# Kernel tuning notes

Hardware: AMD Instinct MI355X
Metric: run time of the kernel (lower is better)

## Reference

```python
import jax, jax.numpy as jnp
import numpy as np

N = 8192      # points
K = 16        # nsample neighbors
CIN = 64      # in_plane
C = 256       # out_plane (== mid_planes)
S = 8         # share_planes
EPS = 1e-5


def _bn(x, g, b, axes):
    # BatchNorm1d (training-mode batch stats, biased var), channel = last dim
    m = x.mean(axes, keepdims=True)
    v = x.var(axes, keepdims=True)
    return (x - m) / jnp.sqrt(v + EPS) * g + b


def _knn(p, k):
    # brute-force KNN over a single batch (o = [N]); indices include self
    sq = jnp.sum(p * p, axis=1)
    d2 = sq[:, None] + sq[None, :] - 2.0 * (p @ p.T)   # [N, N]
    idx = jax.lax.top_k(-d2, k)[1]                      # [N, K]
    return jax.lax.stop_gradient(idx)


def setup_inputs() -> dict:
    key = jax.random.key(0)
    ks = jax.random.split(key, 16)
    W = lambda i, shp, s=0.05: jax.random.normal(ks[i], shp, jnp.float32) * s
    one = lambda d: jnp.ones((d,), jnp.float32)
    zero = lambda d: jnp.zeros((d,), jnp.float32)
    return {
        "p": jax.random.normal(ks[0], (N, 3), jnp.float32),
        "x": jax.random.normal(ks[1], (N, CIN), jnp.float32),
        "o": jnp.array([N], dtype=jnp.int32),
        # PointAggregation (stride=1): Linear(no bias) + BN
        "W_pa": W(2, (CIN, C)), "g_pa": one(C), "b_pa": zero(C),
        # SelfFusion.linear1 (no bias) + bn1
        "W1": W(3, (C, C)), "g1": one(C), "b1": zero(C),
        # SelfFusionLayer q/k/v
        "Wq": W(4, (C, C)), "bq": zero(C),
        "Wk": W(5, (C, C)), "bk": zero(C),
        "Wv": W(6, (C, C)), "bv": zero(C),
        # linear_p: Linear(3,3)+BN(3)+ReLU+Linear(3,C)
        "Wp1": W(7, (3, 3), 0.3), "bp1": zero(3), "gp": one(3), "bp": zero(3),
        "Wp2": W(8, (3, C), 0.3), "bp2": zero(C),
        # linear_w: BN(C)+ReLU+Linear(C,C//S)+BN(C//S)+ReLU+Linear(C//S,C//S)
        "gw1": one(C), "bw1": zero(C),
        "Ww1": W(9, (C, C // S)), "bww1": zero(C // S),
        "gw2": one(C // S), "bw2": zero(C // S),
        "Ww2": W(10, (C // S, C // S), 0.2), "bww2": zero(C // S),
        # bn2, linear3 (no bias) + bn3
        "g2": one(C), "b2": zero(C),
        "W3": W(11, (C, C)), "g3": one(C), "b3": zero(C),
    }


def reference(p, x, o, W_pa, g_pa, b_pa, W1, g1, b1, Wq, bq, Wk, bk, Wv, bv,
              Wp1, bp1, gp, bp, Wp2, bp2, gw1, bw1, Ww1, bww1, gw2, bw2,
              Ww2, bww2, g2, b2, W3, g3, b3):
    relu = jax.nn.relu
    # --- PointAggregation (stride=1) ---
    h = relu(_bn(x @ W_pa, g_pa, b_pa, (0,)))          # [N, C]
    # --- SelfFusion block ---
    identity = h
    h = relu(_bn(h @ W1, g1, b1, (0,)))                # [N, C]
    # SelfFusionLayer
    xq = h @ Wq + bq                                   # [N, C]
    xk = h @ Wk + bk
    xv = h @ Wv + bv
    idx = _knn(p, K)                                   # [N, K]
    rel = p[idx] - p[:, None, :]                       # [N, K, 3] relative coords
    xk_g = xk[idx]                                     # [N, K, C]
    xv_g = xv[idx]                                     # [N, K, C]
    # linear_p: Linear(3,3) -> BN(3) -> ReLU -> Linear(3,C)
    p_r = rel @ Wp1 + bp1
    p_r = relu(_bn(p_r, gp, bp, (0, 1)))
    p_r = p_r @ Wp2 + bp2                              # [N, K, C]
    # mid_planes == out_planes so view(...).sum(2) is identity
    w = xk_g - xq[:, None, :] + p_r                    # [N, K, C]
    # linear_w: BN -> ReLU -> Linear -> BN -> ReLU -> Linear
    w = relu(_bn(w, gw1, bw1, (0, 1)))
    w = w @ Ww1 + bww1                                 # [N, K, C//S]
    w = relu(_bn(w, gw2, bw2, (0, 1)))
    w = w @ Ww2 + bww2                                 # [N, K, C//S]
    w = jax.nn.softmax(w, axis=1)                      # softmax over neighbors
    y = ((xv_g + p_r).reshape(N, K, S, C // S) * w[:, :, None, :]).sum(1)
    y = y.reshape(N, C)
    # back in SelfFusion
    y = relu(_bn(y, g2, b2, (0,)))
    y = _bn(y @ W3, g3, b3, (0,))
    x2 = relu(y + identity)
    return (p, x2, o)
```

## Files before the change

kernel.cpp:

```cpp
#include <hip/hip_runtime.h>
#include <hip/hip_bf16.h>

#define INV_N  (1.0f/8192.0f)
#define INV_NK (1.0f/131072.0f)

typedef __attribute__((ext_vector_type(8))) short bf16x8;
typedef __attribute__((ext_vector_type(4))) float f32x4;
typedef unsigned short u16;

__device__ __forceinline__ u16 f2b(float f) {
  unsigned u = __float_as_uint(f);
  return (u16)((u + 0x7FFFu + ((u >> 16) & 1u)) >> 16);
}
__device__ __forceinline__ float b2f(u16 u) {
  return __uint_as_float(((unsigned)u) << 16);
}

__device__ __forceinline__ float bn_ap(float v, const float* st, int C, int ch,
                                       float inv, float g, float b) {
  float m = st[ch] * inv;
  float var = st[C + ch] * inv - m * m;
  return (v - m) * rsqrtf(var + 1e-5f) * g + b;
}

// ... 111 lines not shown
  float* lscl = (float*)(smem + 18432);
  float* lsft = (float*)(smem + 19456);
  int t = threadIdx.x;
  int m0 = bm * 64, n0 = bn_ * 64;
  if (BNA) {
    for (int e = t; e < KA; e += 256) {
      float m = st[e] * inv_cnt;
      float var = st[KA + e] * inv_cnt - m*m;
      float sc = rsqrtf(var + 1e-5f) * g[e];
      lscl[e] = sc; lsft[e] = bb[e] - m*sc;
    }
    __syncthreads();
  }
  const f32x4 zero = {0.f, 0.f, 0.f, 0.f};
  f32x4 acc[2][2] = {{zero, zero}, {zero, zero}};
  int wv = t >> 6, l = t & 63;
  int wm = wv & 1, wn = wv >> 1;
  int lr = l & 15, lk = (l >> 4) * 8;
  int ra = t >> 4, qa = t & 15;
  int bn = t & 63, bkc = t >> 6;
  for (int k0 = 0; k0 < KA; k0 += 64) {
#pragma unroll
    for (int rp = 0; rp < 4; ++rp) {
      int r = rp*16 + ra;
      float vv[4];
      if constexpr (sizeof(TA) == 4) {
        float4 av = *(const float4*)((const float*)A + (size_t)(m0 + r)*KA + k0 + qa*4);
        vv[0] = av.x; vv[1] = av.y; vv[2] = av.z; vv[3] = av.w;
      } else {
        short4 av = *(const short4*)((const u16*)A + (size_t)(m0 + r)*KA + k0 + qa*4);
#pragma unroll
        for (int jj = 0; jj < 4; ++jj) vv[jj] = b2f(((u16*)&av)[jj]);
      }
      short4 s;
#pragma unroll
      for (int jj = 0; jj < 4; ++jj) {
        float v = vv[jj];
        if (BNA) { int ch = k0 + qa*4 + jj; v = fmaxf(fmaf(v, lscl[ch], lsft[ch]), 0.f); }
        ((u16*)&s)[jj] = f2b(v);
      }
      *(short4*)&As[r][qa*4] = s;
    }
    {
      float v[16];
#pragma unroll
      for (int j2 = 0; j2 < 16; ++j2)
        v[j2] = W[(size_t)(k0 + bkc*16 + j2)*NOUT + n0 + bn];
      bf16x8 w0, w1v;
#pragma unroll
      for (int j2 = 0; j2 < 8; ++j2) {
        w0[j2]  = (short)f2b(v[j2]);
        w1v[j2] = (short)f2b(v[8 + j2]);
      }
      *(bf16x8*)&Bt[bn][bkc*16]     = w0;
      *(bf16x8*)&Bt[bn][bkc*16 + 8] = w1v;
    }
    __syncthreads();
#pragma unroll
    for (int fk = 0; fk < 2; ++fk) {
      bf16x8 a0 = *(const bf16x8*)&As[wm*32 +      lr][fk*32 + lk];
      bf16x8 a1 = *(const bf16x8*)&As[wm*32 + 16 + lr][fk*32 + lk];
      bf16x8 b0 = *(const bf16x8*)&Bt[wn*32 +      lr][fk*32 + lk];
      bf16x8 b1 = *(const bf16x8*)&Bt[wn*32 + 16 + lr][fk*32 + lk];
      acc[0][0] = __builtin_amdgcn_mfma_f32_16x16x32_bf16(a0, b0, acc[0][0], 0, 0, 0);
      acc[0][1] = __builtin_amdgcn_mfma_f32_16x16x32_bf16(a0, b1, acc[0][1], 0, 0, 0);
      acc[1][0] = __builtin_amdgcn_mfma_f32_16x16x32_bf16(a1, b0, acc[1][0], 0, 0, 0);
      acc[1][1] = __builtin_amdgcn_mfma_f32_16x16x32_bf16(a1, b1, acc[1][1], 0, 0, 0);
    }
    __syncthreads();
  }
#pragma unroll
  for (int fn = 0; fn < 2; ++fn) {
    int col = n0 + wn*32 + fn*16 + lr;
    float s1 = 0.f, s2 = 0.f;
#pragma unroll
    for (int fm = 0; fm < 2; ++fm) {
#pragma unroll
      for (int r = 0; r < 4; ++r) {
        int row = m0 + wm*32 + fm*16 + (l >> 4)*4 + r;
        float v = acc[fm][fn][r];
        if constexpr (sizeof(TO) == 4) out[(size_t)row*NOUT + col] = v;
        else                           out[(size_t)row*NOUT + col] = f2b(v);
        if (STATS) { s1 += v; s2 += v*v; }
      }
    }
    if (STATS) {
      s1 += __shfl_xor(s1, 16); s1 += __shfl_xor(s1, 32);
      s2 += __shfl_xor(s2, 16); s2 += __shfl_xor(s2, 32);
      if (l < 16) {
        atomicAdd(&stout[col], s1);
        atomicAdd(&stout[NOUT + col], s2);
      }
    }
  }
}

__device__ __forceinline__ void comp_pr1(const float* p, int i, int j,
                                         const float* Wp1, const float* bp1,
                                         float pr1[3]) {
  float rx = p[j*3+0] - p[i*3+0];
  float ry = p[j*3+1] - p[i*3+1];
  float rz = p[j*3+2] - p[i*3+2];
#pragma unroll
  for (int c = 0; c < 3; ++c)
    pr1[c] = rx*Wp1[c] + ry*Wp1[3+c] + rz*Wp1[6+c] + bp1[c];
}

__device__ __forceinline__ void comp_prv(const float* p, int i, int j,
                                         const float* Wp1, const float* bp1,
                                         const float* gp, const float* bpp,
                                         const float* sp, float o3[3]) {
  float pr1[3];
  comp_pr1(p, i, j, Wp1, bp1, pr1);
#pragma unroll
  for (int c = 0; c < 3; ++c)
    o3[c] = fmaxf(bn_ap(pr1[c], sp, 3, c, INV_NK, gp[c], bpp[c]), 0.0f);
}

__device__ __forceinline__ void prstats_dev(char* smem,
    const float* __restrict__ p, const int* __restrict__ idx,
    const float* Wp1, const float* bp1, float* __restrict__ sp, int pb) {
  float s[3] = {0,0,0}, s2[3] = {0,0,0};
  for (int it = 0; it < 4; ++it) {
    int e = pb*1024 + it*256 + threadIdx.x;
    int i = e >> 4;
    int j = idx[e] & 8191;
    float pr1[3];
    comp_pr1(p, i, j, Wp1, bp1, pr1);
#pragma unroll
    for (int c = 0; c < 3; ++c) { s[c] += pr1[c]; s2[c] += pr1[c]*pr1[c]; }
  }
#pragma unroll
  for (int m = 1; m < 64; m <<= 1) {
#pragma unroll
    for (int c = 0; c < 3; ++c) {
      s[c]  += __shfl_xor(s[c],  m);
      s2[c] += __shfl_xor(s2[c], m);
    }
  }
  float (*red)[6] = (float(*)[6])smem;
  int wv = threadIdx.x >> 6, lane = threadIdx.x & 63;
  if (lane == 0) {
#pragma unroll
    for (int c = 0; c < 3; ++c) { red[wv][c] = s[c]; red[wv][3+c] = s2[c]; }
  }
  __syncthreads();
  if (threadIdx.x < 6) {
    float v = red[0][threadIdx.x] + red[1][threadIdx.x] +
              red[2][threadIdx.x] + red[3][threadIdx.x];
    atomicAdd(&sp[threadIdx.x], v);
  }
}

__launch_bounds__(256)
__global__ void gemmknn_k(const float* __restrict__ x, const float* __restrict__ W_pa,
                          u16* __restrict__ t0, float* __restrict__ st0,
                          const float4* __restrict__ pp, int* __restrict__ idxo) {
  extern __shared__ char smem[];
  int b = blockIdx.x;
  if (b < 512)
    mfgemm_dev<float, u16, false, true>(smem, x, nullptr, nullptr, nullptr, 0.f,
                                        W_pa, t0, st0, 64, 256, b & 127, b >> 7);
  else
    knn_dev(smem, pp, idxo, b - 512);
}

__launch_bounds__(256)
__global__ void gemmpr_k(const u16* __restrict__ t0, const float* __restrict__ st0,
                         const float* __restrict__ g_pa, const float* __restrict__ b_pa,
                         const float* __restrict__ W1, u16* __restrict__ t1,
                         float* __restrict__ st1,
                         const float* __restrict__ p, const int* __restrict__ idx,
                         const float* __restrict__ Wp1, const float* __restrict__ bp1,
                         float* __restrict__ sp) {
  extern __shared__ char smem[];
  int b = blockIdx.x;
  if (b < 512)
    mfgemm_dev<u16, u16, true, true>(smem, t0, st0, g_pa, b_pa, INV_N,
                                     W1, t1, st1, 256, 256, b & 127, b >> 7);
  else
    prstats_dev(smem, p, idx, Wp1, bp1, sp, b - 512);
}

template<typename TA, typename TO, bool BNA, bool STATS>
__launch_bounds__(256)
__global__ void mfgemm_k(const TA* __restrict__ A, const float* __restrict__ st,
                         const float* __restrict__ g, const float* __restrict__ bb,
                         float inv_cnt,
                         const float* __restrict__ W, TO* __restrict__ out,
                         float* __restrict__ stout, int KA, int NOUT) {
  extern __shared__ char smem[];
  mfgemm_dev<TA, TO, BNA, STATS>(smem, A, st, g, bb, inv_cnt, W, out, stout,
                                 KA, NOUT, blockIdx.x, blockIdx.y);
}

__launch_bounds__(256)
__global__ void qkv_k(const u16* __restrict__ t1, const float* __restrict__ st,
                      const float* __restrict__ g1, const float* __restrict__ b1,
                      const float* __restrict__ Wq, const float* __restrict__ bq,
                      const float* __restrict__ Wk, const float* __restrict__ bk,
                      const float* __restrict__ Wv, const float* __restrict__ bv,
                      u16* __restrict__ xq, u16* __restrict__ xk, u16* __restrict__ xv) {
  __shared__ short As[64][72];
  __shared__ short Bt[3][64][72];
  __shared__ float lscl[256], lsft[256];
  int t = threadIdx.x;
  int m0 = blockIdx.x * 64, n0 = blockIdx.y * 64;
  {
    int e = t;
    float m = st[e] * INV_N;
    float var = st[256 + e] * INV_N - m*m;
    float sc = rsqrtf(var + 1e-5f) * g1[e];
    lscl[e] = sc; lsft[e] = b1[e] - m*sc;
  }
  __syncthreads();
  const f32x4 zero = {0.f, 0.f, 0.f, 0.f};
  f32x4 acc[3][2][2];
#pragma unroll
  for (int w = 0; w < 3; ++w)
#pragma unroll
    for (int i = 0; i < 2; ++i)
#pragma unroll
      for (int j = 0; j < 2; ++j) acc[w][i][j] = zero;
  int wv = t >> 6, l = t & 63;
  int wm = wv & 1, wn = wv >> 1;
  int lr = l & 15, lk = (l >> 4) * 8;
  int ra = t >> 4, qa = t & 15;
  int bn = t & 63, bkc = t >> 6;
  const float* Ws[3] = {Wq, Wk, Wv};
  for (int k0 = 0; k0 < 256; k0 += 64) {
#pragma unroll
    for (int rp = 0; rp < 4; ++rp) {
      int r = rp*16 + ra;
      short4 av = *(const short4*)(t1 + (size_t)(m0 + r)*256 + k0 + qa*4);
      short4 s;
#pragma unroll
      for (int jj = 0; jj < 4; ++jj) {
        int ch = k0 + qa*4 + jj;
        float v = fmaxf(fmaf(b2f(((u16*)&av)[jj]), lscl[ch], lsft[ch]), 0.f);
        ((u16*)&s)[jj] = f2b(v);
      }
      *(short4*)&As[r][qa*4] = s;
    }
#pragma unroll
    for (int w = 0; w < 3; ++w) {
      float v[16];
#pragma unroll
      for (int j2 = 0; j2 < 16; ++j2)
        v[j2] = Ws[w][(size_t)(k0 + bkc*16 + j2)*256 + n0 + bn];
      bf16x8 w0, w1v;
#pragma unroll
      for (int j2 = 0; j2 < 8; ++j2) {
        w0[j2]  = (short)f2b(v[j2]);
        w1v[j2] = (short)f2b(v[8 + j2]);
      }
      *(bf16x8*)&Bt[w][bn][bkc*16]     = w0;
      *(bf16x8*)&Bt[w][bn][bkc*16 + 8] = w1v;
    }
    __syncthreads();
#pragma unroll
    for (int fk = 0; fk < 2; ++fk) {
      bf16x8 a0 = *(const bf16x8*)&As[wm*32 +      lr][fk*32 + lk];
      bf16x8 a1 = *(const bf16x8*)&As[wm*32 + 16 + lr][fk*32 + lk];
#pragma unroll
      for (int w = 0; w < 3; ++w) {
        bf16x8 b0 = *(const bf16x8*)&Bt[w][wn*32 +      lr][fk*32 + lk];
        bf16x8 b1 = *(const bf16x8*)&Bt[w][wn*32 + 16 + lr][fk*32 + lk];
        acc[w][0][0] = __builtin_amdgcn_mfma_f32_16x16x32_bf16(a0, b0, acc[w][0][0], 0, 0, 0);
        acc[w][0][1] = __builtin_amdgcn_mfma_f32_16x16x32_bf16(a0, b1, acc[w][0][1], 0, 0, 0);
        acc[w][1][0] = __builtin_amdgcn_mfma_f32_16x16x32_bf16(a1, b0, acc[w][1][0], 0, 0, 0);
        acc[w][1][1] = __builtin_amdgcn_mfma_f32_16x16x32_bf16(a1, b1, acc[w][1][1], 0, 0, 0);
      }
    }
    __syncthreads();
  }
  u16* outs[3] = {xq, xk, xv};
  const float* bs[3] = {bq, bk, bv};
#pragma unroll
  for (int w = 0; w < 3; ++w) {
#pragma unroll
    for (int fn = 0; fn < 2; ++fn) {
      int col = n0 + wn*32 + fn*16 + lr;
      float bvv = bs[w][col];
#pragma unroll
      for (int fm = 0; fm < 2; ++fm) {
#pragma unroll
        for (int r = 0; r < 4; ++r) {
          int row = m0 + wm*32 + fm*16 + (l >> 4)*4 + r;
          outs[w][(size_t)row*256 + col] = f2b(acc[w][fm][fn][r] + bvv);
        }
      }
    }
  }
}

__launch_bounds__(256)
__global__ void stats256_k(const u16* __restrict__ X, float* __restrict__ psy) {
  int c = threadIdx.x;
  int r0 = blockIdx.x * 32;
  float s1 = 0.f, s2 = 0.f;
  for (int r = 0; r < 32; ++r) {
    float v = b2f(X[(size_t)(r0 + r)*256 + c]);
    s1 += v; s2 += v*v;
  }
  psy[(size_t)blockIdx.x*512 + c]       = s1;
  psy[(size_t)blockIdx.x*512 + 256 + c] = s2;
}

__launch_bounds__(256)
__global__ void wstats_k(const u16* __restrict__ xk, const u16* __restrict__ xq,
                         const float* __restrict__ p, const int* __restrict__ idx,
                         const float* Wp1, const float* bp1, const float* gp, const float* bpp,
                         const float* sp, const float* __restrict__ Wp2, const float* bp2,
                         float* __restrict__ pws) {
  __shared__ float prv[8][16][4];
  __shared__ int   jidx[8][16];
  int base = blockIdx.x * 8;
  int t = threadIdx.x;
  if (t < 128) {
    int pt = t >> 4, k = t & 15;
    int j = idx[(base + pt)*16 + k] & 8191;
    jidx[pt][k] = j;
    float o3[3];
    comp_prv(p, base + pt, j, Wp1, bp1, gp, bpp, sp, o3);
    prv[pt][k][0] = o3[0]; prv[pt][k][1] = o3[1]; prv[pt][k][2] = o3[2];
  }
  __syncthreads();
  int c = t;
  float wp0 = Wp2[c], wp1v = Wp2[256+c], wp2v = Wp2[512+c];
  float bbv = bp2[c];
  float s1 = 0.f, s2 = 0.f;
  for (int pt = 0; pt < 8; ++pt) {
    int i = base + pt;
    float xqv = b2f(xq[(size_t)i*256 + c]);
    u16 kvals[16];
#pragma unroll
    for (int k = 0; k < 16; ++k)
      kvals[k] = xk[(size_t)jidx[pt][k]*256 + c];
#pragma unroll
    for (int k = 0; k < 16; ++k) {
      float pr = prv[pt][k][0]*wp0 + prv[pt][k][1]*wp1v + prv[pt][k][2]*wp2v + bbv;
      float wval = b2f(kvals[k]) - xqv + pr;
      s1 += wval; s2 += wval*wval;
    }
  }
  pws[(size_t)blockIdx.x*512 + c]       = s1;
  pws[(size_t)blockIdx.x*512 + 256 + c] = s2;
}

__launch_bounds__(256)
__global__ void w1gemm_k(const u16* __restrict__ xk, const u16* __restrict__ xq,
                         const float* __restrict__ p, const int* __restrict__ idx,
                         const float* Wp1, const float* bp1, const float* gp, const float* bpp,
                         const float* sp, const float* __restrict__ Wp2, const float* bp2,
                         const float* sw, const float* gw1, const float* bw1,
                         const u16* __restrict__ Ww1t, const float* bww1,
                         u16* __restrict__ w1, float* __restrict__ pw1) {
  __shared__ short sA[64][264];
  __shared__ float prv[64][3];
  __shared__ int   jrow[64];
  __shared__ float sred[256];
  int t = threadIdx.x;
  int base4 = blockIdx.x * 4;
  if (t < 64) {
    int grow = blockIdx.x*64 + t;
    int j = idx[grow] & 8191;
    jrow[t] = j;
    float o3[3];
    comp_prv(p, grow >> 4, j, Wp1, bp1, gp, bpp, sp, o3);
    prv[t][0] = o3[0]; prv[t][1] = o3[1]; prv[t][2] = o3[2];
  }
  __syncthreads();
  {
    int o = t & 31, rs = t >> 5;
    int ch0 = o*8;
    int jr[8];
#pragma unroll
    for (int ii = 0; ii < 8; ++ii) jr[ii] = jrow[ii*8 + rs];
    bf16x8 kvv[8], qvv[8];
#pragma unroll
    for (int ii = 0; ii < 8; ++ii) {
      int r = ii*8 + rs;
      kvv[ii] = *(const bf16x8*)(xk + (size_t)jr[ii]*256 + ch0);
      qvv[ii] = *(const bf16x8*)(xq + (size_t)(base4 + (r >> 4))*256 + ch0);
    }
    float sclv[8], sftv[8], w0v[8], w1vv[8], w2v[8], b2v[8];
#pragma unroll
    for (int h = 0; h < 2; ++h) {
      float4 swm = *(const float4*)(sw + ch0 + h*4);
      float4 sws = *(const float4*)(sw + 256 + ch0 + h*4);
      float4 g4  = *(const float4*)(gw1 + ch0 + h*4);
      float4 bb4 = *(const float4*)(bw1 + ch0 + h*4);
      float4 p0v = *(const float4*)(Wp2 + ch0 + h*4);
      float4 p1v = *(const float4*)(Wp2 + 256 + ch0 + h*4);
      float4 p2v = *(const float4*)(Wp2 + 512 + ch0 + h*4);
      float4 bp4 = *(const float4*)(bp2 + ch0 + h*4);
      float mv[4] = {swm.x, swm.y, swm.z, swm.w};
      float sv[4] = {sws.x, sws.y, sws.z, sws.w};
      float gv[4] = {g4.x, g4.y, g4.z, g4.w};
      float bv[4] = {bb4.x, bb4.y, bb4.z, bb4.w};
      float a0[4] = {p0v.x, p0v.y, p0v.z, p0v.w};
      float a1[4] = {p1v.x, p1v.y, p1v.z, p1v.w};
      float a2[4] = {p2v.x, p2v.y, p2v.z, p2v.w};
      float a3[4] = {bp4.x, bp4.y, bp4.z, bp4.w};
#pragma unroll
      for (int jj = 0; jj < 4; ++jj) {
        int e = h*4 + jj;
        float m = mv[jj]*INV_NK;
        float var = sv[jj]*INV_NK - m*m;
        float sc = rsqrtf(var + 1e-5f)*gv[jj];
        sclv[e] = sc; sftv[e] = bv[jj] - m*sc;
        w0v[e] = a0[jj]; w1vv[e] = a1[jj]; w2v[e] = a2[jj]; b2v[e] = a3[jj];
      }
    }
#pragma unroll
    for (int ii = 0; ii < 8; ++ii) {
      int r = ii*8 + rs;
      float p0 = prv[r][0], p1 = prv[r][1], p2 = prv[r][2];
      bf16x8 av;
#pragma unroll
      for (int e = 0; e < 8; ++e) {
        float v = b2f((u16)kvv[ii][e]) - b2f((u16)qvv[ii][e])
                + p0*w0v[e] + p1*w1vv[e] + p2*w2v[e] + b2v[e];
        v = fmaxf(fmaf(v, sclv[e], sftv[e]), 0.f);
        av[e] = (short)f2b(v);
      }
      *(bf16x8*)&sA[r][ch0] = av;
    }
  }
  __syncthreads();
  const f32x4 zero = {0.f,0.f,0.f,0.f};
  f32x4 acc[2] = {zero, zero};
  int wv = t >> 6, l = t & 63;
  int lr = l & 15, hi = l >> 4;
#pragma unroll
  for (int k0 = 0; k0 < 8; ++k0) {
    int kb = k0*32 + hi*8;
    bf16x8 a  = *(const bf16x8*)&sA[wv*16 + lr][kb];
    bf16x8 b0 = *(const bf16x8*)(Ww1t + (size_t)lr*256      + kb);
    bf16x8 b1 = *(const bf16x8*)(Ww1t + (size_t)(16+lr)*256 + kb);
    acc[0] = __builtin_amdgcn_mfma_f32_16x16x32_bf16(a, b0, acc[0], 0, 0, 0);
    acc[1] = __builtin_amdgcn_mfma_f32_16x16x32_bf16(a, b1, acc[1], 0, 0, 0);
  }
#pragma unroll
  for (int fn = 0; fn < 2; ++fn) {
    int col = fn*16 + lr;
    float bv = bww1[col];
    float s1 = 0.f, s2 = 0.f;
#pragma unroll
    for (int r = 0; r < 4; ++r) {
      int grow = blockIdx.x*64 + wv*16 + hi*4 + r;
      float v = acc[fn][r] + bv;
      w1[(size_t)grow*32 + col] = f2b(v);
      s1 += v; s2 += v*v;
    }
    s1 += __shfl_xor(s1, 16); s1 += __shfl_xor(s1, 32);
    s2 += __shfl_xor(s2, 16); s2 += __shfl_xor(s2, 32);
    if (l < 16) { sred[(wv*2+fn)*16 + lr] = s1; sred[128 + (wv*2+fn)*16 + lr] = s2; }
  }
  __syncthreads();
  if (t < 32) {
    float a = 0.f, b = 0.f;
#pragma unroll
    for (int w2 = 0; w2 < 4; ++w2) {
      a += sred[(w2*2 + (t >> 4))*16 + (t & 15)];
      b += sred[128 + (w2*2 + (t >> 4))*16 + (t & 15)];
    }
    pw1[(size_t)blockIdx.x*64 + t]      = a;
    pw1[(size_t)blockIdx.x*64 + 32 + t] = b;
  }
}

__launch_bounds__(256)
__global__ void aggr_k(const u16* __restrict__ w1, const float* sw1,
                       const float* gw2, const float* bw2,
                       const float* __restrict__ Ww2, const float* bww2,
                       const u16* __restrict__ xv,
                       const float* __restrict__ p, const int* __restrict__ idx,
                       const float* Wp1, const float* bp1, const float* gp, const float* bpp,
                       const float* sp, const float* __restrict__ Wp2, const float* bp2,
                       u16* __restrict__ y) {
  __shared__ float lw1[16][32];
  __shared__ float lW2[32][32];
  __shared__ float sw2[16][33];
  __shared__ float prv[16][4];
  __shared__ int   jidx[16];
  int i = blockIdx.x, t = threadIdx.x;
  for (int e = t; e < 1024; e += 256) lW2[e >> 5][e & 31] = Ww2[e];
  for (int e = t; e < 512; e += 256) {
    int c32 = e & 31;
    float v = b2f(w1[(size_t)i*512 + e]);
    v = fmaxf(bn_ap(v, sw1, 32, c32, INV_NK, gw2[c32], bw2[c32]), 0.0f);
    lw1[e >> 5][c32] = v;
  }
  if (t < 16) jidx[t] = idx[i*16 + t] & 8191;
  __syncthreads();
  if (t < 16) {
    float o3[3];
    comp_prv(p, i, jidx[t], Wp1, bp1, gp, bpp, sp, o3);
    prv[t][0] = o3[0]; prv[t][1] = o3[1]; prv[t][2] = o3[2];
  }
  for (int e = t; e < 512; e += 256) {
    int k = e >> 5, c32 = e & 31;
    float a = bww2[c32];
#pragma unroll
    for (int j = 0; j < 32; ++j) a += lw1[k][j] * lW2[j][c32];
    sw2[k][c32] = a;
  }
  __syncthreads();
  if (t < 32) {
    float mx = -3.0e38f;
#pragma unroll
    for (int k = 0; k < 16; ++k) mx = fmaxf(mx, sw2[k][t]);
    float s = 0.f;
#pragma unroll
    for (int k = 0; k < 16; ++k) { float e2 = expf(sw2[k][t] - mx); sw2[k][t] = e2; s += e2; }
    float r = 1.0f / s;
#pragma unroll
    for (int k = 0; k < 16; ++k) sw2[k][t] *= r;
  }
  __syncthreads();
  int c = t;
  float wp0 = Wp2[c], wp1v = Wp2[256+c], wp2v = Wp2[512+c];
  float bbv = bp2[c];
  int c32 = c & 31;
  float acc = 0.f;
#pragma unroll
  for (int k = 0; k < 16; ++k) {
    int j = jidx[k];
    float pr = prv[k][0]*wp0 + prv[k][1]*wp1v + prv[k][2]*wp2v + bbv;
    float xvv = b2f(xv[(size_t)j*256 + c]);
    acc += (xvv + pr) * sw2[k][c32];
  }
  y[(size_t)i*256 + c] = f2b(acc);
}

__launch_bounds__(256)
__global__ void final_k(const u16* __restrict__ t0, const float* s0,
                        const float* g0, const float* b0,
                        const u16* __restrict__ t3, const float* s3,
                        const float* g3, const float* b3,
                        float* __restrict__ out) {
  int i = blockIdx.x, c = threadIdx.x;
  size_t off = (size_t)i*256 + c;
  float h0 = fmaxf(bn_ap(b2f(t0[off]), s0, 256, c, INV_N, g0[c], b0[c]), 0.0f);
  float v3 = bn_ap(b2f(t3[off]), s3, 256, c, INV_N, g3[c], b3[c]);
  out[24576 + off] = fmaxf(v3 + h0, 0.0f);
}

extern "C" void kernel_launch(void* const* d_in, const int* in_sizes, int n_in,
                              void* d_out, int out_size, void* d_ws, size_t ws_size,
                              hipStream_t stream) {
  (void)in_sizes; (void)n_in; (void)out_size; (void)ws_size;
  const float* p    = (const float*)d_in[0];
  const float* x    = (const float*)d_in[1];
  const int*   o    = (const int*)  d_in[2];
  const float* W_pa = (const float*)d_in[3];
  const float* g_pa = (const float*)d_in[4];
  const float* b_pa = (const float*)d_in[5];
  const float* W1   = (const float*)d_in[6];
  const float* g1   = (const float*)d_in[7];
  const float* b1   = (const float*)d_in[8];
  const float* Wq   = (const float*)d_in[9];
  const float* bq   = (const float*)d_in[10];
  const float* Wk   = (const float*)d_in[11];
  const float* bk   = (const float*)d_in[12];
  const float* Wv   = (const float*)d_in[13];
  const float* bv   = (const float*)d_in[14];
  const float* Wp1  = (const float*)d_in[15];
  const float* bp1  = (const float*)d_in[16];
  const float* gp   = (const float*)d_in[17];
  const float* bpp  = (const float*)d_in[18];
  const float* Wp2  = (const float*)d_in[19];
  const float* bp2  = (const float*)d_in[20];
  const float* gw1  = (const float*)d_in[21];
  const float* bw1  = (const float*)d_in[22];
  const float* Ww1  = (const float*)d_in[23];
  const float* bww1 = (const float*)d_in[24];
  const float* gw2  = (const float*)d_in[25];
  const float* bw2  = (const float*)d_in[26];
  const float* Ww2  = (const float*)d_in[27];
  const float* bww2 = (const float*)d_in[28];
  const float* g2   = (const float*)d_in[29];
  const float* b2   = (const float*)d_in[30];
  const float* W3   = (const float*)d_in[31];
  const float* g3   = (const float*)d_in[32];
  const float* b3   = (const float*)d_in[33];

  char* ws = (char*)d_ws;
  u16*   t0  = (u16*)  (ws + 0);
  u16*   t1  = (u16*)  (ws + 4194304);
  u16*   xq  = (u16*)  (ws + 8388608);
  u16*   xk  = (u16*)  (ws + 12582912);
  u16*   xv  = (u16*)  (ws + 16777216);
  u16*   w1  = (u16*)  (ws + 20971520);
  int*   idx = (int*)  (ws + 29360128);
  float* st  = (float*)(ws + 29884416);
  u16*   Ww1t= (u16*)  (ws + 29900800);
  float* pw1 = (float*)(ws + 30408704);
  float* pws = (float*)(ws + 30932992);
  float* psy = (float*)(ws + 33030144);
  u16*   y   = t1;
  u16*   t3  = xq;
  float4* pp = (float4*)(ws + 20971520);

  prep_k<<<96, 256, 0, stream>>>(p, o, Ww1, pp, Ww1t, st, (float*)d_out);

  gemmknn_k<<<1536, 256, 32768, stream>>>(x, W_pa, t0, st + 0, pp, idx);

  gemmpr_k<<<640, 256, 20480, stream>>>(t0, st + 0, g_pa, b_pa, W1, t1, st + 512,
                                        p, idx, Wp1, bp1, st + 2624);

  qkv_k<<<dim3(128, 4), 256, 0, stream>>>(
      t1, st + 512, g1, b1, Wq, bq, Wk, bk, Wv, bv, xq, xk, xv);

  wstats_k<<<1024, 256, 0, stream>>>(xk, xq, p, idx, Wp1, bp1, gp, bpp,
                                     st + 2624, Wp2, bp2, pws);
  red_k<1024, 4><<<32, 256, 0, stream>>>(pws, st + 1024, 512);

  w1gemm_k<<<2048, 256, 0, stream>>>(xk, xq, p, idx, Wp1, bp1, gp, bpp,
                                     st + 2624, Wp2, bp2, st + 1024,
                                     gw1, bw1, Ww1t, bww1, w1, pw1);
  red_k<2048, 16><<<16, 256, 0, stream>>>(pw1, st + 2560, 64);

  aggr_k<<<8192, 256, 0, stream>>>(w1, st + 2560, gw2, bw2, Ww2, bww2, xv,
                                   p, idx, Wp1, bp1, gp, bpp, st + 2624,
                                   Wp2, bp2, y);
  stats256_k<<<256, 256, 0, stream>>>(y, psy);
  red_k<256, 2><<<16, 256, 0, stream>>>(psy, st + 1536, 512);

  mfgemm_k<u16, u16, true, true><<<dim3(128, 4), 256, 20480, stream>>>(
      y, st + 1536, g2, b2, INV_N, W3, t3, st + 2048, 256, 256);

  final_k<<<8192, 256, 0, stream>>>(t0, st + 0, g_pa, b_pa,
                                    t3, st + 2048, g3, b3, (float*)d_out);
}
```

Measured before the change: 188.5 us.

## Rebalance KNN across two fused launches, fuse QKV with pr-stats, wave-per-point aggregation

```diff
diff --git a/kernel.cpp b/kernel.cpp
--- a/kernel.cpp
+++ b/kernel.cpp
@@ -287,6 +287,108 @@
   }
 }
 
+__device__ __forceinline__ void qkv_dev(char* smem,
+    const u16* __restrict__ t1, const float* __restrict__ st,
+    const float* __restrict__ g1, const float* __restrict__ b1,
+    const float* __restrict__ Wq, const float* __restrict__ bq,
+    const float* __restrict__ Wk, const float* __restrict__ bk,
+    const float* __restrict__ Wv, const float* __restrict__ bv,
+    u16* __restrict__ xq, u16* __restrict__ xk, u16* __restrict__ xv_,
+    int bm, int bn_) {
+  short (*As)[72] = (short(*)[72])smem;
+  short (*Bt)[64][72] = (short(*)[64][72])(smem + 9216);
+  float* lscl = (float*)(smem + 36864);
+  float* lsft = (float*)(smem + 37888);
+  int t = threadIdx.x;
+  int m0 = bm * 64, n0 = bn_ * 64;
+  {
+    int e = t;
+    float m = st[e] * INV_N;
+    float var = st[256 + e] * INV_N - m*m;
+    float sc = rsqrtf(var + 1e-5f) * g1[e];
+    lscl[e] = sc; lsft[e] = b1[e] - m*sc;
+  }
+  __syncthreads();
+  const f32x4 zero = {0.f, 0.f, 0.f, 0.f};
+  f32x4 acc[3][2][2];
+#pragma unroll
+  for (int w = 0; w < 3; ++w)
+#pragma unroll
+    for (int i = 0; i < 2; ++i)
+#pragma unroll
+      for (int j = 0; j < 2; ++j) acc[w][i][j] = zero;
+  int wv = t >> 6, l = t & 63;
+  int wm = wv & 1, wn = wv >> 1;
+  int lr = l & 15, lk = (l >> 4) * 8;
+  int ra = t >> 4, qa = t & 15;
+  int bn = t & 63, bkc = t >> 6;
+  const float* Ws[3] = {Wq, Wk, Wv};
+  for (int k0 = 0; k0 < 256; k0 += 64) {
+#pragma unroll
+    for (int rp = 0; rp < 4; ++rp) {
+      int r = rp*16 + ra;
+      short4 av = *(const short4*)(t1 + (size_t)(m0 + r)*256 + k0 + qa*4);
+      short4 s;
+#pragma unroll
+      for (int jj = 0; jj < 4; ++jj) {
+        int ch = k0 + qa*4 + jj;
+        float v = fmaxf(fmaf(b2f(((u16*)&av)[jj]), lscl[ch], lsft[ch]), 0.f);
+        ((u16*)&s)[jj] = f2b(v);
+      }
+      *(short4*)&As[r][qa*4] = s;
+    }
+#pragma unroll
+    for (int w = 0; w < 3; ++w) {
+      float v[16];
+#pragma unroll
+      for (int j2 = 0; j2 < 16; ++j2)
+        v[j2] = Ws[w][(size_t)(k0 + bkc*16 + j2)*256 + n0 + bn];
+      bf16x8 w0, w1v;
+#pragma unroll
+      for (int j2 = 0; j2 < 8; ++j2) {
+        w0[j2]  = (short)f2b(v[j2]);
+        w1v[j2] = (short)f2b(v[8 + j2]);
+      }
+      *(bf16x8*)&Bt[w][bn][bkc*16]     = w0;
+      *(bf16x8*)&Bt[w][bn][bkc*16 + 8] = w1v;
+    }
+    __syncthreads();
+#pragma unroll
+    for (int fk = 0; fk < 2; ++fk) {
+      bf16x8 a0 = *(const bf16x8*)&As[wm*32 +      lr][fk*32 + lk];
+      bf16x8 a1 = *(const bf16x8*)&As[wm*32 + 16 + lr][fk*32 + lk];
+#pragma unroll
+      for (int w = 0; w < 3; ++w) {
+        bf16x8 b0 = *(const bf16x8*)&Bt[w][wn*32 +      lr][fk*32 + lk];
+        bf16x8 b1 = *(const bf16x8*)&Bt[w][wn*32 + 16 + lr][fk*32 + lk];
+        acc[w][0][0] = __builtin_amdgcn_mfma_f32_16x16x32_bf16(a0, b0, acc[w][0][0], 0, 0, 0);
+        acc[w][0][1] = __builtin_amdgcn_mfma_f32_16x16x32_bf16(a0, b1, acc[w][0][1], 0, 0, 0);
+        acc[w][1][0] = __builtin_amdgcn_mfma_f32_16x16x32_bf16(a1, b0, acc[w][1][0], 0, 0, 0);
+        acc[w][1][1] = __builtin_amdgcn_mfma_f32_16x16x32_bf16(a1, b1, acc[w][1][1], 0, 0, 0);
+      }
+    }
+    __syncthreads();
+  }
+  u16* outs[3] = {xq, xk, xv_};
+  const float* bs[3] = {bq, bk, bv};
+#pragma unroll
+  for (int w = 0; w < 3; ++w) {
+#pragma unroll
+    for (int fn = 0; fn < 2; ++fn) {
+      int col = n0 + wn*32 + fn*16 + lr;
+      float bvv = bs[w][col];
+#pragma unroll
+      for (int fm = 0; fm < 2; ++fm) {
+#pragma unroll
+        for (int r = 0; r < 4; ++r) {
+          int row = m0 + wm*32 + fm*16 + (l >> 4)*4 + r;
+          outs[w][(size_t)row*256 + col] = f2b(acc[w][fm][fn][r] + bvv);
+        }
+      }
+    }
+  }
+}
+
 __launch_bounds__(256)
 __global__ void gemmknn_k(const float* __restrict__ x, const float* __restrict__ W_pa,
                           u16* __restrict__ t0, float* __restrict__ st0,
@@ -305,14 +407,31 @@
                          const float* __restrict__ g_pa, const float* __restrict__ b_pa,
                          const float* __restrict__ W1, u16* __restrict__ t1,
                          float* __restrict__ st1,
-                         const float* __restrict__ p, const int* __restrict__ idx,
-                         const float* __restrict__ Wp1, const float* __restrict__ bp1,
-                         float* __restrict__ sp) {
+                         const float4* __restrict__ pp, int* __restrict__ idxo) {
   extern __shared__ char smem[];
   int b = blockIdx.x;
   if (b < 512)
     mfgemm_dev<u16, u16, true, true>(smem, t0, st0, g_pa, b_pa, INV_N,
                                      W1, t1, st1, 256, 256, b & 127, b >> 7);
+  else
+    knn_dev(smem, pp, idxo, b);
+}
+
+__launch_bounds__(256)
+__global__ void qkvpr_k(const u16* __restrict__ t1, const float* __restrict__ st1,
+                        const float* __restrict__ g1, const float* __restrict__ b1,
+                        const float* __restrict__ Wq, const float* __restrict__ bq,
+                        const float* __restrict__ Wk, const float* __restrict__ bk,
+                        const float* __restrict__ Wv, const float* __restrict__ bv,
+                        u16* __restrict__ xq, u16* __restrict__ xk, u16* __restrict__ xv,
+                        const float* __restrict__ p, const int* __restrict__ idx,
+                        const float* __restrict__ Wp1, const float* __restrict__ bp1,
+                        float* __restrict__ sp) {
+  extern __shared__ char smem[];
+  int b = blockIdx.x;
+  if (b < 512)
+    qkv_dev(smem, t1, st1, g1, b1, Wq, bq, Wk, bk, Wv, bv, xq, xk, xv,
+            b & 127, b >> 7);
   else
     prstats_dev(smem, p, idx, Wp1, bp1, sp, b - 512);
 }
@@ -327,106 +446,6 @@
   extern __shared__ char smem[];
   mfgemm_dev<TA, TO, BNA, STATS>(smem, A, st, g, bb, inv_cnt, W, out, stout,
                                  KA, NOUT, blockIdx.x, blockIdx.y);
-}
-
-__launch_bounds__(256)
-__global__ void qkv_k(const u16* __restrict__ t1, const float* __restrict__ st,
-                      const float* __restrict__ g1, const float* __restrict__ b1,
-                      const float* __restrict__ Wq, const float* __restrict__ bq,
-                      const float* __restrict__ Wk, const float* __restrict__ bk,
-                      const float* __restrict__ Wv, const float* __restrict__ bv,
-                      u16* __restrict__ xq, u16* __restrict__ xk, u16* __restrict__ xv) {
-  __shared__ short As[64][72];
-  __shared__ short Bt[3][64][72];
-  __shared__ float lscl[256], lsft[256];
-  int t = threadIdx.x;
-  int m0 = blockIdx.x * 64, n0 = blockIdx.y * 64;
-  {
-    int e = t;
-    float m = st[e] * INV_N;
-    float var = st[256 + e] * INV_N - m*m;
-    float sc = rsqrtf(var + 1e-5f) * g1[e];
-    lscl[e] = sc; lsft[e] = b1[e] - m*sc;
-  }
-  __syncthreads();
-  const f32x4 zero = {0.f, 0.f, 0.f, 0.f};
-  f32x4 acc[3][2][2];
-#pragma unroll
-  for (int w = 0; w < 3; ++w)
-#pragma unroll
-    for (int i = 0; i < 2; ++i)
-#pragma unroll
-      for (int j = 0; j < 2; ++j) acc[w][i][j] = zero;
-  int wv = t >> 6, l = t & 63;
-  int wm = wv & 1, wn = wv >> 1;
-  int lr = l & 15, lk = (l >> 4) * 8;
-  int ra = t >> 4, qa = t & 15;
-  int bn = t & 63, bkc = t >> 6;
-  const float* Ws[3] = {Wq, Wk, Wv};
-  for (int k0 = 0; k0 < 256; k0 += 64) {
-#pragma unroll
-    for (int rp = 0; rp < 4; ++rp) {
-      int r = rp*16 + ra;
-      short4 av = *(const short4*)(t1 + (size_t)(m0 + r)*256 + k0 + qa*4);
-      short4 s;
-#pragma unroll
-      for (int jj = 0; jj < 4; ++jj) {
-        int ch = k0 + qa*4 + jj;
-        float v = fmaxf(fmaf(b2f(((u16*)&av)[jj]), lscl[ch], lsft[ch]), 0.f);
-        ((u16*)&s)[jj] = f2b(v);
-      }
-      *(short4*)&As[r][qa*4] = s;
-    }
-#pragma unroll
-    for (int w = 0; w < 3; ++w) {
-      float v[16];
-#pragma unroll
-      for (int j2 = 0; j2 < 16; ++j2)
-        v[j2] = Ws[w][(size_t)(k0 + bkc*16 + j2)*256 + n0 + bn];
-      bf16x8 w0, w1v;
-#pragma unroll
-      for (int j2 = 0; j2 < 8; ++j2) {
-        w0[j2]  = (short)f2b(v[j2]);
-        w1v[j2] = (short)f2b(v[8 + j2]);
-      }
-      *(bf16x8*)&Bt[w][bn][bkc*16]     = w0;
-      *(bf16x8*)&Bt[w][bn][bkc*16 + 8] = w1v;
-    }
-    __syncthreads();
-#pragma unroll
-    for (int fk = 0; fk < 2; ++fk) {
-      bf16x8 a0 = *(const bf16x8*)&As[wm*32 +      lr][fk*32 + lk];
-      bf16x8 a1 = *(const bf16x8*)&As[wm*32 + 16 + lr][fk*32 + lk];
-#pragma unroll
-      for (int w = 0; w < 3; ++w) {
-        bf16x8 b0 = *(const bf16x8*)&Bt[w][wn*32 +      lr][fk*32 + lk];
-        bf16x8 b1 = *(const bf16x8*)&Bt[w][wn*32 + 16 + lr][fk*32 + lk];
-        acc[w][0][0] = __builtin_amdgcn_mfma_f32_16x16x32_bf16(a0, b0, acc[w][0][0], 0, 0, 0);
-        acc[w][0][1] = __builtin_amdgcn_mfma_f32_16x16x32_bf16(a0, b1, acc[w][0][1], 0, 0, 0);
-        acc[w][1][0] = __builtin_amdgcn_mfma_f32_16x16x32_bf16(a1, b0, acc[w][1][0], 0, 0, 0);
-        acc[w][1][1] = __builtin_amdgcn_mfma_f32_16x16x32_bf16(a1, b1, acc[w][1][1], 0, 0, 0);
-      }
-    }
-    __syncthreads();
-  }
-  u16* outs[3] = {xq, xk, xv};
-  const float* bs[3] = {bq, bk, bv};
-#pragma unroll
-  for (int w = 0; w < 3; ++w) {
-#pragma unroll
-    for (int fn = 0; fn < 2; ++fn) {
-      int col = n0 + wn*32 + fn*16 + lr;
-      float bvv = bs[w][col];
-#pragma unroll
-      for (int fm = 0; fm < 2; ++fm) {
-#pragma unroll
-        for (int r = 0; r < 4; ++r) {
-          int row = m0 + wm*32 + fm*16 + (l >> 4)*4 + r;
-          outs[w][(size_t)row*256 + col] = f2b(acc[w][fm][fn][r] + bvv);
-        }
-      }
-    }
-  }
 }
 
 __launch_bounds__(256)
@@ -615,59 +634,75 @@
                        const float* Wp1, const float* bp1, const float* gp, const float* bpp,
                        const float* sp, const float* __restrict__ Wp2, const float* bp2,
                        u16* __restrict__ y) {
-  __shared__ float lw1[16][32];
   __shared__ float lW2[32][32];
-  __shared__ float sw2[16][33];
-  __shared__ float prv[16][4];
-  __shared__ int   jidx[16];
-  int i = blockIdx.x, t = threadIdx.x;
+  __shared__ float lw1s[4][16][33];
+  __shared__ float swn[4][16][33];
+  __shared__ float prv[4][16][3];
+  __shared__ int   jidx[4][16];
+  int t = threadIdx.x;
+  int wv = t >> 6, lane = t & 63;
+  int i = blockIdx.x*4 + wv;
   for (int e = t; e < 1024; e += 256) lW2[e >> 5][e & 31] = Ww2[e];
-  for (int e = t; e < 512; e += 256) {
-    int c32 = e & 31;
-    float v = b2f(w1[(size_t)i*512 + e]);
-    v = fmaxf(bn_ap(v, sw1, 32, c32, INV_NK, gw2[c32], bw2[c32]), 0.0f);
-    lw1[e >> 5][c32] = v;
-  }
-  if (t < 16) jidx[t] = idx[i*16 + t] & 8191;
+  if (t < 64) {
+    int q = blockIdx.x*4 + (t >> 4);
+    int j = idx[q*16 + (t & 15)] & 8191;
+    jidx[t >> 4][t & 15] = j;
+    float o3[3];
+    comp_prv(p, q, j, Wp1, bp1, gp, bpp, sp, o3);
+    prv[t>>4][t&15][0] = o3[0];
+    prv[t>>4][t&15][1] = o3[1];
+    prv[t>>4][t&15][2] = o3[2];
+  }
+  {
+    bf16x8 v8 = *(const bf16x8*)(w1 + (size_t)i*512 + lane*8);
+#pragma unroll
+    for (int e = 0; e < 8; ++e) {
+      int e512 = lane*8 + e;
+      int k = e512 >> 5, j = e512 & 31;
+      float v = fmaxf(bn_ap(b2f((u16)v8[e]), sw1, 32, j, INV_NK, gw2[j], bw2[j]), 0.0f);
+      lw1s[wv][k][j] = v;
+    }
+  }
   __syncthreads();
-  if (t < 16) {
-    float o3[3];
-    comp_prv(p, i, jidx[t], Wp1, bp1, gp, bpp, sp, o3);
-    prv[t][0] = o3[0]; prv[t][1] = o3[1]; prv[t][2] = o3[2];
-  }
-  for (int e = t; e < 512; e += 256) {
-    int k = e >> 5, c32 = e & 31;
+  int c32 = lane & 31, h = lane >> 5;
+  float sv[8];
+#pragma unroll
+  for (int kk = 0; kk < 8; ++kk) {
+    int k = h*8 + kk;
     float a = bww2[c32];
 #pragma unroll
-    for (int j = 0; j < 32; ++j) a += lw1[k][j] * lW2[j][c32];
-    sw2[k][c32] = a;
-  }
+    for (int j = 0; j < 32; ++j) a += lw1s[wv][k][j] * lW2[j][c32];
+    sv[kk] = a;
+  }
+  float mx = sv[0];
+#pragma unroll
+  for (int kk = 1; kk < 8; ++kk) mx = fmaxf(mx, sv[kk]);
+  mx = fmaxf(mx, __shfl_xor(mx, 32));
+  float s = 0.f;
+#pragma unroll
+  for (int kk = 0; kk < 8; ++kk) { sv[kk] = expf(sv[kk] - mx); s += sv[kk]; }
+  s += __shfl_xor(s, 32);
+  float r = 1.0f / s;
+#pragma unroll
+  for (int kk = 0; kk < 8; ++kk) swn[wv][h*8 + kk][c32] = sv[kk]*r;
   __syncthreads();
-  if (t < 32) {
-    float mx = -3.0e38f;
-#pragma unroll
-    for (int k = 0; k < 16; ++k) mx = fmaxf(mx, sw2[k][t]);
-    float s = 0.f;
-#pragma unroll
-    for (int k = 0; k < 16; ++k) { float e2 = expf(sw2[k][t] - mx); sw2[k][t] = e2; s += e2; }
-    float r = 1.0f / s;
-#pragma unroll
-    for (int k = 0; k < 16; ++k) sw2[k][t] *= r;
-  }
-  __syncthreads();
-  int c = t;
-  float wp0 = Wp2[c], wp1v = Wp2[256+c], wp2v = Wp2[512+c];
-  float bbv = bp2[c];
-  int c32 = c & 31;
-  float acc = 0.f;
-#pragma unroll
-  for (int k = 0; k < 16; ++k) {
-    int j = jidx[k];
-    float pr = prv[k][0]*wp0 + prv[k][1]*wp1v + prv[k][2]*wp2v + bbv;
-    float xvv = b2f(xv[(size_t)j*256 + c]);
-    acc += (xvv + pr) * sw2[k][c32];
-  }
-  y[(size_t)i*256 + c] = f2b(acc);
+  float wn[16];
+#pragma unroll
+  for (int k = 0; k < 16; ++k) wn[k] = swn[wv][k][lane & 31];
+#pragma unroll
+  for (int m = 0; m < 4; ++m) {
+    int c = lane + m*64;
+    float wp0 = Wp2[c], wp1v = Wp2[256+c], wp2v = Wp2[512+c];
+    float bbv = bp2[c];
+    float acc = 0.f;
+#pragma unroll
+    for (int k = 0; k < 16; ++k) {
+      int j = jidx[wv][k];
+      float pr = prv[wv][k][0]*wp0 + prv[wv][k][1]*wp1v + prv[wv][k][2]*wp2v + bbv;
+      acc += (b2f(xv[(size_t)j*256 + c]) + pr) * wn[k];
+    }
+    y[(size_t)i*256 + c] = f2b(acc);
+  }
 }
 
 __launch_bounds__(256)
@@ -741,13 +776,14 @@
 
   prep_k<<<96, 256, 0, stream>>>(p, o, Ww1, pp, Ww1t, st, (float*)d_out);
 
-  gemmknn_k<<<1536, 256, 32768, stream>>>(x, W_pa, t0, st + 0, pp, idx);
-
-  gemmpr_k<<<640, 256, 20480, stream>>>(t0, st + 0, g_pa, b_pa, W1, t1, st + 512,
-                                        p, idx, Wp1, bp1, st + 2624);
-
-  qkv_k<<<dim3(128, 4), 256, 0, stream>>>(
-      t1, st + 512, g1, b1, Wq, bq, Wk, bk, Wv, bv, xq, xk, xv);
+  gemmknn_k<<<1024, 256, 32768, stream>>>(x, W_pa, t0, st + 0, pp, idx);
+
+  gemmpr_k<<<1024, 256, 32768, stream>>>(t0, st + 0, g_pa, b_pa, W1, t1, st + 512,
+                                         pp, idx);
+
+  qkvpr_k<<<640, 256, 38912, stream>>>(t1, st + 512, g1, b1, Wq, bq, Wk, bk,
+                                       Wv, bv, xq, xk, xv,
+                                       p, idx, Wp1, bp1, st + 2624);
 
   wstats_k<<<1024, 256, 0, stream>>>(xk, xq, p, idx, Wp1, bp1, gp, bpp,
                                      st + 2624, Wp2, bp2, pws);
@@ -758,7 +794,7 @@
                                      gw1, bw1, Ww1t, bww1, w1, pw1);
   red_k<2048, 16><<<16, 256, 0, stream>>>(pw1, st + 2560, 64);
 
-  aggr_k<<<8192, 256, 0, stream>>>(w1, st + 2560, gw2, bw2, Ww2, bww2, xv,
+  aggr_k<<<2048, 256, 0, stream>>>(w1, st + 2560, gw2, bw2, Ww2, bww2, xv,
                                    p, idx, Wp1, bp1, gp, bpp, st + 2624,
                                    Wp2, bp2, y);
   stats256_k<<<256, 256, 0, stream>>>(y, psy);
```

Result: slower. 249.5 us (+32.4%).

## Split KNN across two GEMM launches and fuse QKV with p_r stats

Applied to the files above, without the earlier changes.

```diff
diff --git a/kernel.cpp b/kernel.cpp
--- a/kernel.cpp
+++ b/kernel.cpp
@@ -287,6 +287,108 @@
   }
 }
 
+__device__ __forceinline__ void qkv_dev(char* smem,
+    const u16* __restrict__ t1, const float* __restrict__ st,
+    const float* __restrict__ g1, const float* __restrict__ b1,
+    const float* __restrict__ Wq, const float* __restrict__ bq,
+    const float* __restrict__ Wk, const float* __restrict__ bk,
+    const float* __restrict__ Wv, const float* __restrict__ bv,
+    u16* __restrict__ xq, u16* __restrict__ xk, u16* __restrict__ xv_,
+    int bm, int bn_) {
+  short (*As)[72] = (short(*)[72])smem;
+  short (*Bt)[64][72] = (short(*)[64][72])(smem + 9216);
+  float* lscl = (float*)(smem + 36864);
+  float* lsft = (float*)(smem + 37888);
+  int t = threadIdx.x;
+  int m0 = bm * 64, n0 = bn_ * 64;
+  {
+    int e = t;
+    float m = st[e] * INV_N;
+    float var = st[256 + e] * INV_N - m*m;
+    float sc = rsqrtf(var + 1e-5f) * g1[e];
+    lscl[e] = sc; lsft[e] = b1[e] - m*sc;
+  }
+  __syncthreads();
+  const f32x4 zero = {0.f, 0.f, 0.f, 0.f};
+  f32x4 acc[3][2][2];
+#pragma unroll
+  for (int w = 0; w < 3; ++w)
+#pragma unroll
+    for (int i = 0; i < 2; ++i)
+#pragma unroll
+      for (int j = 0; j < 2; ++j) acc[w][i][j] = zero;
+  int wv = t >> 6, l = t & 63;
+  int wm = wv & 1, wn = wv >> 1;
+  int lr = l & 15, lk = (l >> 4) * 8;
+  int ra = t >> 4, qa = t & 15;
+  int bn = t & 63, bkc = t >> 6;
+  const float* Ws[3] = {Wq, Wk, Wv};
+  for (int k0 = 0; k0 < 256; k0 += 64) {
+#pragma unroll
+    for (int rp = 0; rp < 4; ++rp) {
+      int r = rp*16 + ra;
+      short4 av = *(const short4*)(t1 + (size_t)(m0 + r)*256 + k0 + qa*4);
+      short4 s;
+#pragma unroll
+      for (int jj = 0; jj < 4; ++jj) {
+        int ch = k0 + qa*4 + jj;
+        float v = fmaxf(fmaf(b2f(((u16*)&av)[jj]), lscl[ch], lsft[ch]), 0.f);
+        ((u16*)&s)[jj] = f2b(v);
+      }
+      *(short4*)&As[r][qa*4] = s;
+    }
+#pragma unroll
+    for (int w = 0; w < 3; ++w) {
+      float v[16];
+#pragma unroll
+      for (int j2 = 0; j2 < 16; ++j2)
+        v[j2] = Ws[w][(size_t)(k0 + bkc*16 + j2)*256 + n0 + bn];
+      bf16x8 w0, w1v;
+#pragma unroll
+      for (int j2 = 0; j2 < 8; ++j2) {
+        w0[j2]  = (short)f2b(v[j2]);
+        w1v[j2] = (short)f2b(v[8 + j2]);
+      }
+      *(bf16x8*)&Bt[w][bn][bkc*16]     = w0;
+      *(bf16x8*)&Bt[w][bn][bkc*16 + 8] = w1v;
+    }
+    __syncthreads();
+#pragma unroll
+    for (int fk = 0; fk < 2; ++fk) {
+      bf16x8 a0 = *(const bf16x8*)&As[wm*32 +      lr][fk*32 + lk];
+      bf16x8 a1 = *(const bf16x8*)&As[wm*32 + 16 + lr][fk*32 + lk];
+#pragma unroll
+      for (int w = 0; w < 3; ++w) {
+        bf16x8 b0 = *(const bf16x8*)&Bt[w][wn*32 +      lr][fk*32 + lk];
+        bf16x8 b1 = *(const bf16x8*)&Bt[w][wn*32 + 16 + lr][fk*32 + lk];
+        acc[w][0][0] = __builtin_amdgcn_mfma_f32_16x16x32_bf16(a0, b0, acc[w][0][0], 0, 0, 0);
+        acc[w][0][1] = __builtin_amdgcn_mfma_f32_16x16x32_bf16(a0, b1, acc[w][0][1], 0, 0, 0);
+        acc[w][1][0] = __builtin_amdgcn_mfma_f32_16x16x32_bf16(a1, b0, acc[w][1][0], 0, 0, 0);
+        acc[w][1][1] = __builtin_amdgcn_mfma_f32_16x16x32_bf16(a1, b1, acc[w][1][1], 0, 0, 0);
+      }
+    }
+    __syncthreads();
+  }
+  u16* outs[3] = {xq, xk, xv_};
+  const float* bs[3] = {bq, bk, bv};
+#pragma unroll
+  for (int w = 0; w < 3; ++w) {
+#pragma unroll
+    for (int fn = 0; fn < 2; ++fn) {
+      int col = n0 + wn*32 + fn*16 + lr;
+      float bvv = bs[w][col];
+#pragma unroll
+      for (int fm = 0; fm < 2; ++fm) {
+#pragma unroll
+        for (int r = 0; r < 4; ++r) {
+          int row = m0 + wm*32 + fm*16 + (l >> 4)*4 + r;
+          outs[w][(size_t)row*256 + col] = f2b(acc[w][fm][fn][r] + bvv);
+        }
+      }
+    }
+  }
+}
+
 __launch_bounds__(256)
 __global__ void gemmknn_k(const float* __restrict__ x, const float* __restrict__ W_pa,
                           u16* __restrict__ t0, float* __restrict__ st0,
@@ -305,14 +407,31 @@
                          const float* __restrict__ g_pa, const float* __restrict__ b_pa,
                          const float* __restrict__ W1, u16* __restrict__ t1,
                          float* __restrict__ st1,
-                         const float* __restrict__ p, const int* __restrict__ idx,
-                         const float* __restrict__ Wp1, const float* __restrict__ bp1,
-                         float* __restrict__ sp) {
+                         const float4* __restrict__ pp, int* __restrict__ idxo) {
   extern __shared__ char smem[];
   int b = blockIdx.x;
   if (b < 512)
     mfgemm_dev<u16, u16, true, true>(smem, t0, st0, g_pa, b_pa, INV_N,
                                      W1, t1, st1, 256, 256, b & 127, b >> 7);
+  else
+    knn_dev(smem, pp, idxo, b);
+}
+
+__launch_bounds__(256)
+__global__ void qkvpr_k(const u16* __restrict__ t1, const float* __restrict__ st1,
+                        const float* __restrict__ g1, const float* __restrict__ b1,
+                        const float* __restrict__ Wq, const float* __restrict__ bq,
+                        const float* __restrict__ Wk, const float* __restrict__ bk,
+                        const float* __restrict__ Wv, const float* __restrict__ bv,
+                        u16* __restrict__ xq, u16* __restrict__ xk, u16* __restrict__ xv,
+                        const float* __restrict__ p, const int* __restrict__ idx,
+                        const float* __restrict__ Wp1, const float* __restrict__ bp1,
+                        float* __restrict__ sp) {
+  extern __shared__ char smem[];
+  int b = blockIdx.x;
+  if (b < 512)
+    qkv_dev(smem, t1, st1, g1, b1, Wq, bq, Wk, bk, Wv, bv, xq, xk, xv,
+            b & 127, b >> 7);
   else
     prstats_dev(smem, p, idx, Wp1, bp1, sp, b - 512);
 }
@@ -327,106 +446,6 @@
   extern __shared__ char smem[];
   mfgemm_dev<TA, TO, BNA, STATS>(smem, A, st, g, bb, inv_cnt, W, out, stout,
                                  KA, NOUT, blockIdx.x, blockIdx.y);
-}
-
-__launch_bounds__(256)
-__global__ void qkv_k(const u16* __restrict__ t1, const float* __restrict__ st,
-                      const float* __restrict__ g1, const float* __restrict__ b1,
-                      const float* __restrict__ Wq, const float* __restrict__ bq,
-                      const float* __restrict__ Wk, const float* __restrict__ bk,
-                      const float* __restrict__ Wv, const float* __restrict__ bv,
-                      u16* __restrict__ xq, u16* __restrict__ xk, u16* __restrict__ xv) {
-  __shared__ short As[64][72];
-  __shared__ short Bt[3][64][72];
-  __shared__ float lscl[256], lsft[256];
-  int t = threadIdx.x;
-  int m0 = blockIdx.x * 64, n0 = blockIdx.y * 64;
-  {
-    int e = t;
-    float m = st[e] * INV_N;
-    float var = st[256 + e] * INV_N - m*m;
-    float sc = rsqrtf(var + 1e-5f) * g1[e];
-    lscl[e] = sc; lsft[e] = b1[e] - m*sc;
-  }
-  __syncthreads();
-  const f32x4 zero = {0.f, 0.f, 0.f, 0.f};
-  f32x4 acc[3][2][2];
-#pragma unroll
-  for (int w = 0; w < 3; ++w)
-#pragma unroll
-    for (int i = 0; i < 2; ++i)
-#pragma unroll
-      for (int j = 0; j < 2; ++j) acc[w][i][j] = zero;
-  int wv = t >> 6, l = t & 63;
-  int wm = wv & 1, wn = wv >> 1;
-  int lr = l & 15, lk = (l >> 4) * 8;
-  int ra = t >> 4, qa = t & 15;
-  int bn = t & 63, bkc = t >> 6;
-  const float* Ws[3] = {Wq, Wk, Wv};
-  for (int k0 = 0; k0 < 256; k0 += 64) {
-#pragma unroll
-    for (int rp = 0; rp < 4; ++rp) {
-      int r = rp*16 + ra;
-      short4 av = *(const short4*)(t1 + (size_t)(m0 + r)*256 + k0 + qa*4);
-      short4 s;
-#pragma unroll
-      for (int jj = 0; jj < 4; ++jj) {
-        int ch = k0 + qa*4 + jj;
-        float v = fmaxf(fmaf(b2f(((u16*)&av)[jj]), lscl[ch], lsft[ch]), 0.f);
-        ((u16*)&s)[jj] = f2b(v);
-      }
-      *(short4*)&As[r][qa*4] = s;
-    }
-#pragma unroll
-    for (int w = 0; w < 3; ++w) {
-      float v[16];
-#pragma unroll
-      for (int j2 = 0; j2 < 16; ++j2)
-        v[j2] = Ws[w][(size_t)(k0 + bkc*16 + j2)*256 + n0 + bn];
-      bf16x8 w0, w1v;
-#pragma unroll
-      for (int j2 = 0; j2 < 8; ++j2) {
-        w0[j2]  = (short)f2b(v[j2]);
-        w1v[j2] = (short)f2b(v[8 + j2]);
-      }
-      *(bf16x8*)&Bt[w][bn][bkc*16]     = w0;
-      *(bf16x8*)&Bt[w][bn][bkc*16 + 8] = w1v;
-    }
-    __syncthreads();
-#pragma unroll
-    for (int fk = 0; fk < 2; ++fk) {
-      bf16x8 a0 = *(const bf16x8*)&As[wm*32 +      lr][fk*32 + lk];
-      bf16x8 a1 = *(const bf16x8*)&As[wm*32 + 16 + lr][fk*32 + lk];
-#pragma unroll
-      for (int w = 0; w < 3; ++w) {
-        bf16x8 b0 = *(const bf16x8*)&Bt[w][wn*32 +      lr][fk*32 + lk];
-        bf16x8 b1 = *(const bf16x8*)&Bt[w][wn*32 + 16 + lr][fk*32 + lk];
-        acc[w][0][0] = __builtin_amdgcn_mfma_f32_16x16x32_bf16(a0, b0, acc[w][0][0], 0, 0, 0);
-        acc[w][0][1] = __builtin_amdgcn_mfma_f32_16x16x32_bf16(a0, b1, acc[w][0][1], 0, 0, 0);
-        acc[w][1][0] = __builtin_amdgcn_mfma_f32_16x16x32_bf16(a1, b0, acc[w][1][0], 0, 0, 0);
-        acc[w][1][1] = __builtin_amdgcn_mfma_f32_16x16x32_bf16(a1, b1, acc[w][1][1], 0, 0, 0);
-      }
-    }
-    __syncthreads();
-  }
-  u16* outs[3] = {xq, xk, xv};
-  const float* bs[3] = {bq, bk, bv};
-#pragma unroll
-  for (int w = 0; w < 3; ++w) {
-#pragma unroll
-    for (int fn = 0; fn < 2; ++fn) {
-      int col = n0 + wn*32 + fn*16 + lr;
-      float bvv = bs[w][col];
-#pragma unroll
-      for (int fm = 0; fm < 2; ++fm) {
-#pragma unroll
-        for (int r = 0; r < 4; ++r) {
-          int row = m0 + wm*32 + fm*16 + (l >> 4)*4 + r;
-          outs[w][(size_t)row*256 + col] = f2b(acc[w][fm][fn][r] + bvv);
-        }
-      }
-    }
-  }
 }
 
 __launch_bounds__(256)
@@ -741,13 +760,14 @@
 
   prep_k<<<96, 256, 0, stream>>>(p, o, Ww1, pp, Ww1t, st, (float*)d_out);
 
-  gemmknn_k<<<1536, 256, 32768, stream>>>(x, W_pa, t0, st + 0, pp, idx);
-
-  gemmpr_k<<<640, 256, 20480, stream>>>(t0, st + 0, g_pa, b_pa, W1, t1, st + 512,
-                                        p, idx, Wp1, bp1, st + 2624);
-
-  qkv_k<<<dim3(128, 4), 256, 0, stream>>>(
-      t1, st + 512, g1, b1, Wq, bq, Wk, bk, Wv, bv, xq, xk, xv);
+  gemmknn_k<<<1024, 256, 32768, stream>>>(x, W_pa, t0, st + 0, pp, idx);
+
+  gemmpr_k<<<1024, 256, 32768, stream>>>(t0, st + 0, g_pa, b_pa, W1, t1, st + 512,
+                                         pp, idx);
+
+  qkvpr_k<<<640, 256, 38912, stream>>>(t1, st + 512, g1, b1, Wq, bq, Wk, bk,
+                                       Wv, bv, xq, xk, xv,
+                                       p, idx, Wp1, bp1, st + 2624);
 
   wstats_k<<<1024, 256, 0, stream>>>(xk, xq, p, idx, Wp1, bp1, gp, bpp,
                                      st + 2624, Wp2, bp2, pws);
```

New measurement: 195.2 us. 3.6% more time.
